# Kernel tuning notes

Measured on AMD Instinct MI355X. Metric: run time of the kernel, lower is better.

The kernel has to match this reference:

```python
import jax, jax.numpy as jnp
import numpy as np

N, E, G = 50000, 800000, 1000
F_IN, H, C = 128, 4, 64  # in-features, heads, per-head channels
NEG_SLOPE = 0.2


def _leaky_relu(v):
    return jnp.where(v > 0, v, NEG_SLOPE * v)


def _gat_conv(x, edge_index, W, a_src, a_dst, bias, heads, out_ch, concat):
    """PyG-style GATConv with add_self_loops=True (eval mode, no dropout)."""
    n = x.shape[0]
    loop = jnp.arange(n, dtype=edge_index.dtype)
    src = jnp.concatenate([edge_index[0], loop])  # [E+N]
    dst = jnp.concatenate([edge_index[1], loop])  # [E+N]
    h = (x @ W).reshape(n, heads, out_ch)          # [N, H, C]
    al_src = jnp.sum(h * a_src, axis=-1)           # [N, H]
    al_dst = jnp.sum(h * a_dst, axis=-1)           # [N, H]
    e = _leaky_relu(al_src[src] + al_dst[dst])     # [E+N, H]
    # segment softmax over incoming edges of each destination node
    m = jax.ops.segment_max(e, dst, num_segments=n)
    ex = jnp.exp(e - jax.lax.stop_gradient(m)[dst])
    denom = jax.ops.segment_sum(ex, dst, num_segments=n)
    alpha = ex / denom[dst]                        # [E+N, H]
    out = jax.ops.segment_sum(h[src] * alpha[..., None], dst, num_segments=n)
    out = out.reshape(n, heads * out_ch) if concat else out.mean(axis=1)
    return out + bias


def _global_mean_pool(x, batch, num_graphs):
    s = jax.ops.segment_sum(x, batch, num_segments=num_graphs)
    cnt = jax.ops.segment_sum(jnp.ones((x.shape[0],), x.dtype), batch, num_segments=num_graphs)
    return s / jnp.maximum(cnt, 1.0)[:, None]


def setup_inputs() -> dict:
    key = jax.random.key(0)
    ks = jax.random.split(key, 20)
    glorot = lambda k, shp: jax.random.normal(k, shp, jnp.float32) * np.sqrt(2.0 / (shp[0] + shp[-1]))
    inp = {
        "x": jax.random.normal(ks[0], (N, F_IN), jnp.float32),
        "edge_index": jax.random.randint(ks[1], (2, E), 0, N, jnp.int32),
        "batch": jnp.sort(jax.random.randint(ks[2], (N,), 0, G, jnp.int32)),
        # conv1: F_IN -> H*C (concat)
        "W1": glorot(ks[3], (F_IN, H * C)),
        "a1_src": glorot(ks[4], (H, C)),
        "a1_dst": glorot(ks[5], (H, C)),
        "b1": jnp.zeros((H * C,), jnp.float32),
        # conv2: H*C -> H*C (concat)
        "W2": glorot(ks[6], (H * C, H * C)),
        "a2_src": glorot(ks[7], (H, C)),
        "a2_dst": glorot(ks[8], (H, C)),
        "b2": jnp.zeros((H * C,), jnp.float32),
        # conv3: H*C -> C (1 head, concat=False)
        "W3": glorot(ks[9], (H * C, C)),
        "a3_src": glorot(ks[10], (1, C)),
        "a3_dst": glorot(ks[11], (1, C)),
        "b3": jnp.zeros((C,), jnp.float32),
        # final linear C -> 1
        "lin_w": glorot(ks[12], (C, 1)),
        "lin_b": jnp.zeros((1,), jnp.float32),
    }
    return inp


def reference(x, edge_index, batch, W1, a1_src, a1_dst, b1, W2, a2_src, a2_dst, b2,
              W3, a3_src, a3_dst, b3, lin_w, lin_b):
    h = jax.nn.elu(_gat_conv(x, edge_index, W1, a1_src, a1_dst, b1, H, C, True))
    h = jax.nn.elu(_gat_conv(h, edge_index, W2, a2_src, a2_dst, b2, H, C, True))
    h = _gat_conv(h, edge_index, W3, a3_src, a3_dst, b3, 1, C, False)
    g = _global_mean_pool(h, batch, G)  # [G, C]
    return g @ lin_w + lin_b            # [G, 1]
```

## Files before the change

### kernel.cpp

```cpp
#include <hip/hip_runtime.h>
#include <cstdint>
#include <cstddef>

#define NEG_SLOPE 0.2f

typedef __attribute__((ext_vector_type(8))) short short8;
typedef __attribute__((ext_vector_type(4))) float f32x4;

__device__ __forceinline__ float lrelu(float v) { return v > 0.f ? v : NEG_SLOPE * v; }

__device__ __forceinline__ unsigned short f2bf(float x) {
    unsigned u = __float_as_uint(x);
    u = (u + 0x7FFFu + ((u >> 16) & 1u)) >> 16;
    return (unsigned short)u;
}
__device__ __forceinline__ float bf2f(unsigned short h) {
    return __uint_as_float(((unsigned)h) << 16);
}

__device__ __forceinline__ void splitbf(float v, unsigned short& hb, unsigned short& lb) {
    unsigned u = __float_as_uint(v);
    hb = (unsigned short)(u >> 16);
    float hf = __uint_as_float(u & 0xFFFF0000u);
    float lf = v - hf;
    lb = (unsigned short)(__float_as_uint(lf) >> 16);
}

__global__ void k_count(const int* __restrict__ ei, int E, int* __restrict__ counts) {
    int i = blockIdx.x * blockDim.x + threadIdx.x;
    if (i < E) atomicAdd(&counts[ei[E + i]], 1);
}

__global__ __launch_bounds__(256) void k_scan_local(const int* __restrict__ counts,
        int* __restrict__ local_ex, int* __restrict__ bsums, int Nn) {
    int base = blockIdx.x * 1024;
    int tid = threadIdx.x;
    int idx = base + tid * 4;
    int4 v = make_int4(0, 0, 0, 0);
    if (idx + 3 < Nn) {
        v = *reinterpret_cast<const int4*>(&counts[idx]);
    } else {
        if (idx + 0 < Nn) v.x = counts[idx + 0];
        if (idx + 1 < Nn) v.y = counts[idx + 1];
        if (idx + 2 < Nn) v.z = counts[idx + 2];
        if (idx + 3 < Nn) v.w = counts[idx + 3];
    }
    int t = v.x + v.y + v.z + v.w;
    int lane = tid & 63, wave = tid >> 6;
    int s = t;
    #pragma unroll
    for (int off = 1; off < 64; off <<= 1) {
        int u = __shfl_up(s, off);
        if (lane >= off) s += u;
    }
    __shared__ int wsum[4];
    if (lane == 63) wsum[wave] = s;
    __syncthreads();
    int wo = 0;
    #pragma unroll
    for (int wv = 0; wv < 4; ++wv) wo += (wv < wave) ? wsum[wv] : 0;
    int ex = wo + s - t;
    int4 o;
    o.x = ex; o.y = ex + v.x; o.z = ex + v.x + v.y; o.w = ex + v.x + v.y + v.z;
    if (idx + 3 < Nn) {
        *reinterpret_cast<int4*>(&local_ex[idx]) = o;
    } else {
        if (idx + 0 < Nn) local_ex[idx + 0] = o.x;
        if (idx + 1 < Nn) local_ex[idx + 1] = o.y;
        if (idx + 2 < Nn) local_ex[idx + 2] = o.z;
        if (idx + 3 < Nn) local_ex[idx + 3] = o.w;
    }
    if (tid == 255) bsums[blockIdx.x] = wo + s;
}

__global__ __launch_bounds__(256) void k_scan_add(const int* __restrict__ local_ex,
        const int* __restrict__ bsums, int* __restrict__ indptr, int* __restrict__ cursor,
        int Nn, int Etot, int NB) {
    __shared__ int pref[64];
    int tid = threadIdx.x;
    if (tid < 64) {
        int v = (tid < NB) ? bsums[tid] : 0;
        int s = v;
        #pragma unroll
        for (int off = 1; off < 64; off <<= 1) {
            int u = __shfl_up(s, off);
            if ((tid & 63) >= off) s += u;
        }
        pref[tid] = s - v;
    }
    __syncthreads();
    int i = blockIdx.x * 256 + tid;
    if (i < Nn) {
        int val = local_ex[i] + pref[i >> 10];
        indptr[i] = val;
        cursor[i] = val;
    } else if (i == Nn) {
        indptr[Nn] = Etot;
    }
}

__global__ void k_scatter(const int* __restrict__ ei, int E, int* __restrict__ cursor,
                          int* __restrict__ csr_src) {
    int i = blockIdx.x * blockDim.x + threadIdx.x;
    if (i < E) {
        int s = ei[i], d = ei[E + i];
        int pos = atomicAdd(&cursor[d], 1);
        csr_src[pos] = s;
    }
}

__device__ __forceinline__ void packB_one(const float* __restrict__ W,
        unsigned short* __restrict__ Ph, unsigned short* __restrict__ Pl,
        int K, int M, int tid) {
    int KS8 = K >> 3;
    int col = tid / KS8;
    int k = (tid - col * KS8) << 3;
    short8 hv, lv;
    #pragma unroll
    for (int j = 0; j < 8; ++j) {
        float x = W[(size_t)(k + j) * M + col];
        unsigned short hb = f2bf(x);
        hv[j] = (short)hb;
        lv[j] = (short)f2bf(x - bf2f(hb));
    }
    int ct64 = col >> 6, c = col & 63;
    int fb = c >> 4, cl = c & 15;
    int ks = k >> 5, kg = (k >> 3) & 3;
    int lane = cl | (kg << 4);
    size_t off = (((size_t)ct64 * (K >> 5) + ks) * 4 + fb) * 64 + lane;
    *reinterpret_cast<short8*>(Ph + off * 8) = hv;
    *reinterpret_cast<short8*>(Pl + off * 8) = lv;
}

__global__ __launch_bounds__(256) void k_packB3(const float* __restrict__ W1,
        const float* __restrict__ W2, const float* __restrict__ W3,
        unsigned short* p1h, unsigned short* p1l,
        unsigned short* p2h, unsigned short* p2l,
        unsigned short* p3h, unsigned short* p3l) {
    int tid = blockIdx.x * 256 + threadIdx.x;
    if (tid < 4096)        packB_one(W1, p1h, p1l, 128, 256, tid);
    else if (tid < 12288)  packB_one(W2, p2h, p2l, 256, 256, tid - 4096);
    else if (tid < 14336)  packB_one(W3, p3h, p3l, 256, 64, tid - 12288);
}

template<int AF, int WR, int WC, bool CONV, int K>
__global__ __launch_bounds__(256) void k_mm(const float* __restrict__ A,
        const unsigned short* __restrict__ Aph, const unsigned short* __restrict__ Apl,
        const unsigned short* __restrict__ Bh, const unsigned short* __restrict__ Bl,
        unsigned short* __restrict__ C, const float* __restrict__ a_src, const float* __restrict__ a_dst,
        float* __restrict__ al_s, float* __restrict__ al_d, int Nrows, int M) {
    constexpr int BF = 4;
    constexpr int BR = WR * AF * 16;
    constexpr int KS = K >> 5;
    int wave = threadIdx.x >> 6, lane = threadIdx.x & 63;
    int wr = wave / WC, wc = wave % WC;
    int rt = blockIdx.x;
    int ct64 = blockIdx.y * WC + wc;
    int rl = lane & 15, kg = lane >> 4;
    const short8* B8h = reinterpret_cast<const short8*>(Bh);
    const short8* B8l = reinterpret_cast<const short8*>(Bl);

    const float* aptr[AF];
    const unsigned short *ahp[AF], *alp[AF];
    #pragma unroll
    for (int f = 0; f < AF; ++f) {
        int row = rt * BR + wr * (AF * 16) + f * 16 + rl;
        if (row > Nrows - 1) row = Nrows - 1;
        if constexpr (CONV) {
            aptr[f] = A + (size_t)row * K + kg * 8;
        } else {
            ahp[f] = Aph + (size_t)row * K + kg * 8;
            alp[f] = Apl + (size_t)row * K + kg * 8;
        }
    }

    f32x4 acc[AF][BF];
    #pragma unroll
    for (int i = 0; i < AF; ++i)
        #pragma unroll
        for (int j = 0; j < BF; ++j)
            acc[i][j] = (f32x4){0.f, 0.f, 0.f, 0.f};

    #pragma unroll
    for (int ks = 0; ks < KS; ++ks) {
        short8 a_h[AF], a_l[AF], b_h[BF], b_l[BF];
        #pragma unroll
        for (int f = 0; f < AF; ++f) {
            if constexpr (CONV) {
                const float* ap = aptr[f] + ks * 32;
                float4 v0 = *reinterpret_cast<const float4*>(ap);
                float4 v1 = *reinterpret_cast<const float4*>(ap + 4);
                float vv[8] = {v0.x, v0.y, v0.z, v0.w, v1.x, v1.y, v1.z, v1.w};
                #pragma unroll
                for (int j = 0; j < 8; ++j) {
                    unsigned short hb, lb;
                    splitbf(vv[j], hb, lb);
                    a_h[f][j] = (short)hb;
                    a_l[f][j] = (short)lb;
                }
            } else {
                a_h[f] = *reinterpret_cast<const short8*>(ahp[f] + ks * 32);
                a_l[f] = *reinterpret_cast<const short8*>(alp[f] + ks * 32);
            }
        }
        #pragma unroll
        for (int f = 0; f < BF; ++f) {
            size_t off = (((size_t)ct64 * KS + ks) * 4 + f) * 64 + lane;
            b_h[f] = B8h[off]; b_l[f] = B8l[off];
        }
        #pragma unroll
        for (int i = 0; i < AF; ++i)
            #pragma unroll
            for (int j = 0; j < BF; ++j) {
                acc[i][j] = __builtin_amdgcn_mfma_f32_16x16x32_bf16(a_l[i], b_h[j], acc[i][j], 0, 0, 0);
                acc[i][j] = __builtin_amdgcn_mfma_f32_16x16x32_bf16(a_h[i], b_l[j], acc[i][j], 0, 0, 0);
                acc[i][j] = __builtin_amdgcn_mfma_f32_16x16x32_bf16(a_h[i], b_h[j], acc[i][j], 0, 0, 0);
            }
    }

    int H = M >> 6;
    int head = ct64;
    int col0 = ct64 * 64;
    int cl = lane & 15, rgrp = lane >> 4;

    float as_[BF], ad_[BF];
    #pragma unroll
    for (int j = 0; j < BF; ++j) {
        as_[j] = a_src[col0 + j * 16 + cl];
        ad_[j] = a_dst[col0 + j * 16 + cl];
    }

    #pragma unroll
    for (int i = 0; i < AF; ++i) {
        int rowb = rt * BR + wr * (AF * 16) + i * 16 + rgrp * 4;
        #pragma unroll
        for (int r = 0; r < 4; ++r) {
            float sv = acc[i][0][r] * as_[0] + acc[i][1][r] * as_[1]
                     + acc[i][2][r] * as_[2] + acc[i][3][r] * as_[3];
            float dv = acc[i][0][r] * ad_[0] + acc[i][1][r] * ad_[1]
                     + acc[i][2][r] * ad_[2] + acc[i][3][r] * ad_[3];
            #pragma unroll
            for (int o = 1; o < 16; o <<= 1) {
                sv += __shfl_xor(sv, o);
                dv += __shfl_xor(dv, o);
            }
            int row = rowb + r;
            if (row < Nrows) {
                unsigned short* cp = &C[(size_t)row * M + col0 + cl];
                cp[0]  = f2bf(acc[i][0][r]);
                cp[16] = f2bf(acc[i][1][r]);
                cp[32] = f2bf(acc[i][2][r]);
                cp[48] = f2bf(acc[i][3][r]);
                if (cl == 0) {
                    al_s[(size_t)row * H + head] = sv;
                    al_d[(size_t)row * H + head] = dv;
                }
            }
        }
    }
}

template <int H, bool ACT, bool POOL>
__global__ __launch_bounds__(256) void k_agg(const unsigned short* __restrict__ hlin,
                      const float* __restrict__ al_s,
                      const float* __restrict__ al_d, const int* __restrict__ indptr,
                      const int* __restrict__ csr_src, const float* __restrict__ bias,
                      unsigned short* __restrict__ out_hi, unsigned short* __restrict__ out_lo,
                      float* __restrict__ outf, const int* __restrict__ batch,
                      int* __restrict__ gcnt, int Nn) {
    constexpr int TOT = H * 64;
    constexpr int VEC = TOT / 64;
    constexpr int CAP = 128;
    constexpr int GRPW = 64 / H;
    __shared__ float sp[4][CAP * H];
    __shared__ int   si[4][CAP];
    int w = threadIdx.x >> 6;
    int lane = threadIdx.x & 63;
    int node = (blockIdx.x * blockDim.x + threadIdx.x) >> 6;
    if (node >= Nn) return;
    int d = node;
    int p0 = indptr[d], p1 = indptr[d + 1];
    int deg = p1 - p0;
    int head = (lane * VEC) >> 6;

    float ad[H], e_self[H];
    if constexpr (H == 4) {
        float4 adv = *reinterpret_cast<const float4*>(&al_d[(size_t)d * 4]);
        float4 asv = *reinterpret_cast<const float4*>(&al_s[(size_t)d * 4]);
        ad[0] = adv.x; ad[1] = adv.y; ad[2] = adv.z; ad[3] = adv.w;
        e_self[0] = lrelu(asv.x + ad[0]); e_self[1] = lrelu(asv.y + ad[1]);
        e_self[2] = lrelu(asv.z + ad[2]); e_self[3] = lrelu(asv.w + ad[3]);
    } else {
        ad[0] = al_d[d];
        e_self[0] = lrelu(al_s[d] + ad[0]);
    }

    if (deg <= CAP) {
        int nb = (deg + 63) >> 6;
        for (int b = 0; b < nb; ++b) {
            int l = b * 64 + lane;
            float e_h[H];
            if (l < deg) {
                int s = csr_src[p0 + l];
                si[w][l] = s;
                if constexpr (H == 4) {
                    float4 sv = *reinterpret_cast<const float4*>(&al_s[(size_t)s * 4]);
                    e_h[0] = lrelu(sv.x + ad[0]); e_h[1] = lrelu(sv.y + ad[1]);
                    e_h[2] = lrelu(sv.z + ad[2]); e_h[3] = lrelu(sv.w + ad[3]);
                } else {
                    e_h[0] = lrelu(al_s[s] + ad[0]);
                }
            } else {
                #pragma unroll
                for (int h = 0; h < H; ++h) e_h[h] = -1e30f;
            }
            #pragma unroll
            for (int h = 0; h < H; ++h) sp[w][l * H + h] = e_h[h];
        }
        int li = lane & (GRPW - 1);
        int tot = nb * 64;
        float mg = e_self[head];
        for (int l = li; l < tot; l += GRPW)
            mg = fmaxf(mg, sp[w][l * H + head]);
        #pragma unroll
        for (int o = 1; o < GRPW; o <<= 1)
            mg = fmaxf(mg, __shfl_xor(mg, o));
        float deng = 0.f;
        for (int l = li; l < tot; l += GRPW) {
            float pv = __expf(sp[w][l * H + head] - mg);
            sp[w][l * H + head] = pv;
            deng += pv;
        }
        #pragma unroll
        for (int o = 1; o < GRPW; o <<= 1)
            deng += __shfl_xor(deng, o);
        float esx = __expf(e_self[head] - mg);
        deng += esx;
        float invden = 1.f / deng;

        float4 accv = make_float4(0.f, 0.f, 0.f, 0.f);
        {
            const unsigned short* hp = hlin + (size_t)d * TOT + lane * VEC;
            if constexpr (VEC == 4) {
                ushort4 hv = *reinterpret_cast<const ushort4*>(hp);
                accv.x = esx * bf2f(hv.x); accv.y = esx * bf2f(hv.y);
                accv.z = esx * bf2f(hv.z); accv.w = esx * bf2f(hv.w);
            } else {
                accv.x = esx * bf2f(hp[0]);
            }
        }
        int e = 0;
        for (; e + 8 <= deg; e += 8) {
            int s0 = si[w][e + 0], s1 = si[w][e + 1], s2 = si[w][e + 2], s3 = si[w][e + 3];
            int s4 = si[w][e + 4], s5 = si[w][e + 5], s6 = si[w][e + 6], s7 = si[w][e + 7];
            float a0 = sp[w][(e + 0) * H + head];
            float a1 = sp[w][(e + 1) * H + head];
            float a2 = sp[w][(e + 2) * H + head];
            float a3 = sp[w][(e + 3) * H + head];
            float a4 = sp[w][(e + 4) * H + head];
            float a5 = sp[w][(e + 5) * H + head];
            float a6 = sp[w][(e + 6) * H + head];
            float a7 = sp[w][(e + 7) * H + head];
            if constexpr (VEC == 4) {
                ushort4 r0 = *reinterpret_cast<const ushort4*>(hlin + (size_t)s0 * TOT + lane * 4);
                ushort4 r1 = *reinterpret_cast<const ushort4*>(hlin + (size_t)s1 * TOT + lane * 4);
                ushort4 r2 = *reinterpret_cast<const ushort4*>(hlin + (size_t)s2 * TOT + lane * 4);
                ushort4 r3 = *reinterpret_cast<const ushort4*>(hlin + (size_t)s3 * TOT + lane * 4);
                ushort4 r4 = *reinterpret_cast<const ushort4*>(hlin + (size_t)s4 * TOT + lane * 4);
                ushort4 r5 = *reinterpret_cast<const ushort4*>(hlin + (size_t)s5 * TOT + lane * 4);
                ushort4 r6 = *reinterpret_cast<const ushort4*>(hlin + (size_t)s6 * TOT + lane * 4);
                ushort4 r7 = *reinterpret_cast<const ushort4*>(hlin + (size_t)s7 * TOT + lane * 4);
                accv.x += a0*bf2f(r0.x) + a1*bf2f(r1.x) + a2*bf2f(r2.x) + a3*bf2f(r3.x)
                        + a4*bf2f(r4.x) + a5*bf2f(r5.x) + a6*bf2f(r6.x) + a7*bf2f(r7.x);
                accv.y += a0*bf2f(r0.y) + a1*bf2f(r1.y) + a2*bf2f(r2.y) + a3*bf2f(r3.y)
                        + a4*bf2f(r4.y) + a5*bf2f(r5.y) + a6*bf2f(r6.y) + a7*bf2f(r7.y);
                accv.z += a0*bf2f(r0.z) + a1*bf2f(r1.z) + a2*bf2f(r2.z) + a3*bf2f(r3.z)
                        + a4*bf2f(r4.z) + a5*bf2f(r5.z) + a6*bf2f(r6.z) + a7*bf2f(r7.z);
                accv.w += a0*bf2f(r0.w) + a1*bf2f(r1.w) + a2*bf2f(r2.w) + a3*bf2f(r3.w)
                        + a4*bf2f(r4.w) + a5*bf2f(r5.w) + a6*bf2f(r6.w) + a7*bf2f(r7.w);
            } else {
                float r0 = bf2f(hlin[(size_t)s0 * TOT + lane]);
                float r1 = bf2f(hlin[(size_t)s1 * TOT + lane]);
                float r2 = bf2f(hlin[(size_t)s2 * TOT + lane]);
                float r3 = bf2f(hlin[(size_t)s3 * TOT + lane]);
                float r4 = bf2f(hlin[(size_t)s4 * TOT + lane]);
                float r5 = bf2f(hlin[(size_t)s5 * TOT + lane]);
                float r6 = bf2f(hlin[(size_t)s6 * TOT + lane]);
                float r7 = bf2f(hlin[(size_t)s7 * TOT + lane]);
                accv.x += a0*r0 + a1*r1 + a2*r2 + a3*r3 + a4*r4 + a5*r5 + a6*r6 + a7*r7;
            }
        }
        for (; e + 4 <= deg; e += 4) {
            int s0 = si[w][e + 0], s1 = si[w][e + 1];
            int s2 = si[w][e + 2], s3 = si[w][e + 3];
            float a0 = sp[w][(e + 0) * H + head];
            float a1 = sp[w][(e + 1) * H + head];
            float a2 = sp[w][(e + 2) * H + head];
            float a3 = sp[w][(e + 3) * H + head];
            if constexpr (VEC == 4) {
                ushort4 r0 = *reinterpret_cast<const ushort4*>(hlin + (size_t)s0 * TOT + lane * 4);
                ushort4 r1 = *reinterpret_cast<const ushort4*>(hlin + (size_t)s1 * TOT + lane * 4);
                ushort4 r2 = *reinterpret_cast<const ushort4*>(hlin + (size_t)s2 * TOT + lane * 4);
                ushort4 r3 = *reinterpret_cast<const ushort4*>(hlin + (size_t)s3 * TOT + lane * 4);
                accv.x += a0*bf2f(r0.x) + a1*bf2f(r1.x) + a2*bf2f(r2.x) + a3*bf2f(r3.x);
                accv.y += a0*bf2f(r0.y) + a1*bf2f(r1.y) + a2*bf2f(r2.y) + a3*bf2f(r3.y);
                accv.z += a0*bf2f(r0.z) + a1*bf2f(r1.z) + a2*bf2f(r2.z) + a3*bf2f(r3.z);
                accv.w += a0*bf2f(r0.w) + a1*bf2f(r1.w) + a2*bf2f(r2.w) + a3*bf2f(r3.w);
            } else {
                float r0 = bf2f(hlin[(size_t)s0 * TOT + lane]);
                float r1 = bf2f(hlin[(size_t)s1 * TOT + lane]);
                float r2 = bf2f(hlin[(size_t)s2 * TOT + lane]);
                float r3 = bf2f(hlin[(size_t)s3 * TOT + lane]);
                accv.x += a0 * r0 + a1 * r1 + a2 * r2 + a3 * r3;
            }
        }
        for (; e < deg; ++e) {
            int s = si[w][e];
            float a = sp[w][e * H + head];
            if constexpr (VEC == 4) {
                ushort4 rv = *reinterpret_cast<const ushort4*>(hlin + (size_t)s * TOT + lane * 4);
                accv.x += a * bf2f(rv.x); accv.y += a * bf2f(rv.y);
                accv.z += a * bf2f(rv.z); accv.w += a * bf2f(rv.w);
            } else {
                accv.x += a * bf2f(hlin[(size_t)s * TOT + lane]);
            }
        }
        if constexpr (VEC == 4) {
            int c0 = lane * 4;
            accv.x = accv.x * invden + bias[c0 + 0];
            accv.y = accv.y * invden + bias[c0 + 1];
            accv.z = accv.z * invden + bias[c0 + 2];
            accv.w = accv.w * invden + bias[c0 + 3];
            if (ACT) {
                accv.x = accv.x > 0.f ? accv.x : expm1f(accv.x);
                accv.y = accv.y > 0.f ? accv.y : expm1f(accv.y);
                accv.z = accv.z > 0.f ? accv.z : expm1f(accv.z);
                accv.w = accv.w > 0.f ? accv.w : expm1f(accv.w);
            }
            ushort4 hv, lv;
            splitbf(accv.x, hv.x, lv.x);
            splitbf(accv.y, hv.y, lv.y);
            splitbf(accv.z, hv.z, lv.z);
            splitbf(accv.w, hv.w, lv.w);
            *reinterpret_cast<ushort4*>(&out_hi[(size_t)d * TOT + c0]) = hv;
            *reinterpret_cast<ushort4*>(&out_lo[(size_t)d * TOT + c0]) = lv;
        } else {
            float o = accv.x * invden + bias[lane];
            if (ACT) o = o > 0.f ? o : expm1f(o);
            if constexpr (POOL) {
                int g = batch[d];
                atomicAdd(&outf[(size_t)g * 64 + lane], o);
                if (lane == 0) atomicAdd(&gcnt[g], 1);
            } else {
                unsigned short hb, lb;
                splitbf(o, hb, lb);
                out_hi[(size_t)d * TOT + lane] = hb;
                out_lo[(size_t)d * TOT + lane] = lb;
            }
        }
        return;
    }

    {
        float adh = ad[head];
        float es = e_self[head];
        float m = es;
        for (int e = p0; e < p1; ++e) {
            int s = csr_src[e];
            m = fmaxf(m, lrelu(al_s[(size_t)s * H + head] + adh));
        }
        float den = __expf(es - m);
        for (int e = p0; e < p1; ++e) {
            int s = csr_src[e];
            den += __expf(lrelu(al_s[(size_t)s * H + head] + adh) - m);
        }
        den = 1.f / den;
        float accv[VEC] = {};
        {
            float alpha = __expf(es - m) * den;
            const unsigned short* hp = hlin + (size_t)d * TOT + lane * VEC;
            #pragma unroll
            for (int v = 0; v < VEC; ++v) accv[v] = alpha * bf2f(hp[v]);
        }
        for (int e = p0; e < p1; ++e) {
            int s = csr_src[e];
            float alpha = __expf(lrelu(al_s[(size_t)s * H + head] + adh) - m) * den;
            const unsigned short* hp = hlin + (size_t)s * TOT + lane * VEC;
            #pragma unroll
            for (int v = 0; v < VEC; ++v) accv[v] += alpha * bf2f(hp[v]);
        }
        #pragma unroll
        for (int v = 0; v < VEC; ++v) {
            int c = lane * VEC + v;
            float o = accv[v] + bias[c];
            if (ACT) o = o > 0.f ? o : expm1f(o);
            accv[v] = o;
        }
        if constexpr (POOL) {
            int g = batch[d];
            atomicAdd(&outf[(size_t)g * 64 + lane], accv[0]);
            if (lane == 0) atomicAdd(&gcnt[g], 1);
        } else {
            #pragma unroll
            for (int v = 0; v < VEC; ++v) {
                unsigned short hb, lb;
                splitbf(accv[v], hb, lb);
                out_hi[(size_t)d * TOT + lane * VEC + v] = hb;
                out_lo[(size_t)d * TOT + lane * VEC + v] = lb;
            }
        }
    }
}

__global__ void k_final(const float* __restrict__ gsum, const int* __restrict__ gcnt,
                        const float* __restrict__ lin_w, const float* __restrict__ lin_b,
                        float* __restrict__ out, int Gn) {
    int g = (blockIdx.x * blockDim.x + threadIdx.x) >> 6;
    int lane = threadIdx.x & 63;
    if (g >= Gn) return;
    float cnt = (float)gcnt[g];
    float inv = 1.f / fmaxf(cnt, 1.f);
    float v = gsum[(size_t)g * 64 + lane] * inv * lin_w[lane];
    #pragma unroll
    for (int off = 32; off >= 1; off >>= 1) v += __shfl_xor(v, off);
    if (lane == 0) out[g] = v + lin_b[0];
}

extern "C" void kernel_launch(void* const* d_in, const int* in_sizes, int n_in,
                              void* d_out, int out_size, void* d_ws, size_t ws_size,
                              hipStream_t stream) {
    const float* x    = (const float*)d_in[0];
    const int*   ei   = (const int*)d_in[1];
    const int*   batch= (const int*)d_in[2];
    const float* W1   = (const float*)d_in[3];
    const float* a1s  = (const float*)d_in[4];
    const float* a1d  = (const float*)d_in[5];
    const float* b1   = (const float*)d_in[6];
    const float* W2   = (const float*)d_in[7];
    const float* a2s  = (const float*)d_in[8];
    const float* a2d  = (const float*)d_in[9];
    const float* b2   = (const float*)d_in[10];
    const float* W3   = (const float*)d_in[11];
    const float* a3s  = (const float*)d_in[12];
    const float* a3d  = (const float*)d_in[13];
    const float* b3   = (const float*)d_in[14];
    const float* lw   = (const float*)d_in[15];
    const float* lb   = (const float*)d_in[16];

    int N = in_sizes[0] / 128;
    int E = in_sizes[1] / 2;
    int G = out_size;
    int RT32 = (N + 31) >> 5;
    int RT64 = (N + 63) >> 6;
    int Np = ((N + 127) >> 7) * 128;
    int NB = (N + 1023) >> 10;

    char* p = (char*)d_ws;
    auto alloc = [&](size_t bytes) {
        char* r = p;
        p += (bytes + 255) & ~(size_t)255;
        return r;
    };
    unsigned short* hbuf = (unsigned short*)alloc((size_t)Np * 256 * 2);
    unsigned short* aggh = (unsigned short*)alloc((size_t)Np * 256 * 2);
    unsigned short* aggl = (unsigned short*)alloc((size_t)Np * 256 * 2);
    unsigned short* pB1h = (unsigned short*)alloc((size_t)128 * 256 * 2);
    unsigned short* pB1l = (unsigned short*)alloc((size_t)128 * 256 * 2);
    unsigned short* pB2h = (unsigned short*)alloc((size_t)256 * 256 * 2);
    unsigned short* pB2l = (unsigned short*)alloc((size_t)256 * 256 * 2);
    unsigned short* pB3h = (unsigned short*)alloc((size_t)256 * 64 * 2);
    unsigned short* pB3l = (unsigned short*)alloc((size_t)256 * 64 * 2);
    float* al_s  = (float*)alloc((size_t)N * 4 * 4);
    float* al_d  = (float*)alloc((size_t)N * 4 * 4);
    int* indptr  = (int*)alloc((size_t)(N + 1) * 4);
    int* counts  = (int*)alloc((size_t)N * 4);
    int* cursor  = (int*)alloc((size_t)N * 4);
    int* lex     = (int*)alloc((size_t)N * 4);
    int* bsums   = (int*)alloc((size_t)256 * 4);
    int* csr     = (int*)alloc((size_t)E * 4);
    float* gsum  = (float*)alloc((size_t)G * 64 * 4);
    int* gcnt    = (int*)alloc((size_t)G * 4);
    if ((size_t)(p - (char*)d_ws) > ws_size) return;

    hipMemsetAsync(counts, 0, (size_t)N * 4, stream);
    hipMemsetAsync(gsum, 0, (size_t)G * 64 * 4, stream);
    hipMemsetAsync(gcnt, 0, (size_t)G * 4, stream);

    k_packB3<<<(14336 + 255) / 256, 256, 0, stream>>>(W1, W2, W3,
        pB1h, pB1l, pB2h, pB2l, pB3h, pB3l);

    int eb = (E + 255) / 256;
    k_count<<<eb, 256, 0, stream>>>(ei, E, counts);
    k_scan_local<<<NB, 256, 0, stream>>>(counts, lex, bsums, N);
    k_scan_add<<<(N + 1 + 255) / 256, 256, 0, stream>>>(lex, bsums, indptr, cursor, N, E, NB);
    k_scatter<<<eb, 256, 0, stream>>>(ei, E, cursor, csr);

    int wb = (N * 64 + 255) / 256;

    k_mm<2, 1, 4, true, 128><<<dim3(RT32, 1), 256, 0, stream>>>(x, nullptr, nullptr,
        pB1h, pB1l, hbuf, a1s, a1d, al_s, al_d, N, 256);
    k_agg<4, true, false><<<wb, 256, 0, stream>>>(hbuf, al_s, al_d, indptr, csr, b1,
        aggh, aggl, nullptr, nullptr, nullptr, N);

    k_mm<2, 1, 4, false, 256><<<dim3(RT32, 1), 256, 0, stream>>>(nullptr, aggh, aggl,
        pB2h, pB2l, hbuf, a2s, a2d, al_s, al_d, N, 256);
    k_agg<4, true, false><<<wb, 256, 0, stream>>>(hbuf, al_s, al_d, indptr, csr, b2,
        aggh, aggl, nullptr, nullptr, nullptr, N);

    k_mm<1, 4, 1, false, 256><<<dim3(RT64, 1), 256, 0, stream>>>(nullptr, aggh, aggl,
        pB3h, pB3l, hbuf, a3s, a3d, al_s, al_d, N, 64);
    k_agg<1, false, true><<<wb, 256, 0, stream>>>(hbuf, al_s, al_d, indptr, csr, b3,
        nullptr, nullptr, gsum, batch, gcnt, N);

    int fb = (G * 64 + 255) / 256;
    k_final<<<fb, 256, 0, stream>>>(gsum, gcnt, lw, lb, (float*)d_out, G);
}
```

Measured before the change: 407.3 us.

## Split GAT aggregation per head with head-major attention logits

The 4-head aggregation kernel is restructured so each wave handles a single (node, head) pair rather than a whole node. Blocks are ordered so consecutive blocks share a head across node pairs, and the attention logits are stored head-major (al_s[head*Npad+row]) to make per-head gathers contiguous. Within a wave, four 16-lane groups each gather a different neighbor's 64-channel head slice and combine via shuffles. The aim is to cut per-wave softmax work and improve cache locality of the gathered features. The cost is four times as many waves, each re-reading the CSR indices and neighbor logits.

```diff
diff --git a/kernel.cpp b/kernel.cpp
--- a/kernel.cpp
+++ b/kernel.cpp
@@ -148,7 +148,7 @@
         const unsigned short* __restrict__ Aph, const unsigned short* __restrict__ Apl,
         const unsigned short* __restrict__ Bh, const unsigned short* __restrict__ Bl,
         unsigned short* __restrict__ C, const float* __restrict__ a_src, const float* __restrict__ a_dst,
-        float* __restrict__ al_s, float* __restrict__ al_d, int Nrows, int M) {
+        float* __restrict__ al_s, float* __restrict__ al_d, int Nrows, int M, int Npad) {
     constexpr int BF = 4;
     constexpr int BR = WR * AF * 16;
     constexpr int KS = K >> 5;
@@ -218,7 +218,6 @@
             }
     }
 
-    int H = M >> 6;
     int head = ct64;
     int col0 = ct64 * 64;
     int cl = lane & 15, rgrp = lane >> 4;
@@ -252,263 +251,218 @@
                 cp[32] = f2bf(acc[i][2][r]);
                 cp[48] = f2bf(acc[i][3][r]);
                 if (cl == 0) {
-                    al_s[(size_t)row * H + head] = sv;
-                    al_d[(size_t)row * H + head] = dv;
+                    al_s[(size_t)head * Npad + row] = sv;
+                    al_d[(size_t)head * Npad + row] = dv;
                 }
             }
         }
     }
 }
 
-template <int H, bool ACT, bool POOL>
-__global__ __launch_bounds__(256) void k_agg(const unsigned short* __restrict__ hlin,
-                      const float* __restrict__ al_s,
-                      const float* __restrict__ al_d, const int* __restrict__ indptr,
-                      const int* __restrict__ csr_src, const float* __restrict__ bias,
-                      unsigned short* __restrict__ out_hi, unsigned short* __restrict__ out_lo,
-                      float* __restrict__ outf, const int* __restrict__ batch,
-                      int* __restrict__ gcnt, int Nn) {
-    constexpr int TOT = H * 64;
-    constexpr int VEC = TOT / 64;
+template <bool ACT>
+__global__ __launch_bounds__(256) void k_agg4(const unsigned short* __restrict__ hlin,
+        const float* __restrict__ al_s, const float* __restrict__ al_d,
+        const int* __restrict__ indptr, const int* __restrict__ csr_src,
+        const float* __restrict__ bias,
+        unsigned short* __restrict__ out_hi, unsigned short* __restrict__ out_lo,
+        int Nn, int Npad) {
     constexpr int CAP = 128;
-    constexpr int GRPW = 64 / H;
-    __shared__ float sp[4][CAP * H];
+    __shared__ float sp[4][CAP];
     __shared__ int   si[4][CAP];
     int w = threadIdx.x >> 6;
     int lane = threadIdx.x & 63;
-    int node = (blockIdx.x * blockDim.x + threadIdx.x) >> 6;
-    if (node >= Nn) return;
-    int d = node;
+    int b = blockIdx.x;
+    int r = b & 7, chunk = b >> 3;
+    int q = r >> 1;
+    int nb = chunk * 2 + (r & 1);
+    int d = nb * 4 + w;
+    if (d >= Nn) return;
     int p0 = indptr[d], p1 = indptr[d + 1];
     int deg = p1 - p0;
-    int head = (lane * VEC) >> 6;
-
-    float ad[H], e_self[H];
-    if constexpr (H == 4) {
-        float4 adv = *reinterpret_cast<const float4*>(&al_d[(size_t)d * 4]);
-        float4 asv = *reinterpret_cast<const float4*>(&al_s[(size_t)d * 4]);
-        ad[0] = adv.x; ad[1] = adv.y; ad[2] = adv.z; ad[3] = adv.w;
-        e_self[0] = lrelu(asv.x + ad[0]); e_self[1] = lrelu(asv.y + ad[1]);
-        e_self[2] = lrelu(asv.z + ad[2]); e_self[3] = lrelu(asv.w + ad[3]);
-    } else {
-        ad[0] = al_d[d];
-        e_self[0] = lrelu(al_s[d] + ad[0]);
-    }
+    float adq = al_d[(size_t)q * Npad + d];
+    float e_self = lrelu(al_s[(size_t)q * Npad + d] + adq);
+    int g = lane >> 4, li = lane & 15;
 
     if (deg <= CAP) {
-        int nb = (deg + 63) >> 6;
-        for (int b = 0; b < nb; ++b) {
-            int l = b * 64 + lane;
-            float e_h[H];
-            if (l < deg) {
-                int s = csr_src[p0 + l];
-                si[w][l] = s;
-                if constexpr (H == 4) {
-                    float4 sv = *reinterpret_cast<const float4*>(&al_s[(size_t)s * 4]);
-                    e_h[0] = lrelu(sv.x + ad[0]); e_h[1] = lrelu(sv.y + ad[1]);
-                    e_h[2] = lrelu(sv.z + ad[2]); e_h[3] = lrelu(sv.w + ad[3]);
-                } else {
-                    e_h[0] = lrelu(al_s[s] + ad[0]);
-                }
-            } else {
-                #pragma unroll
-                for (int h = 0; h < H; ++h) e_h[h] = -1e30f;
+        float m = e_self;
+        for (int l = lane; l < deg; l += 64) {
+            int s = csr_src[p0 + l];
+            si[w][l] = s;
+            float e = lrelu(al_s[(size_t)q * Npad + s] + adq);
+            sp[w][l] = e;
+            m = fmaxf(m, e);
+        }
+        #pragma unroll
+        for (int o = 1; o < 64; o <<= 1) m = fmaxf(m, __shfl_xor(m, o));
+        float den = 0.f;
+        for (int l = lane; l < deg; l += 64) {
+            float pv = __expf(sp[w][l] - m);
+            sp[w][l] = pv;
+            den += pv;
+        }
+        #pragma unroll
+        for (int o = 1; o < 64; o <<= 1) den += __shfl_xor(den, o);
+        float esx = __expf(e_self - m);
+        den += esx;
+        float invden = 1.f / den;
+
+        const unsigned short* base = hlin + q * 64 + li * 4;
+        float4 acc = make_float4(0.f, 0.f, 0.f, 0.f);
+        if (g == 0) {
+            ushort4 hv = *reinterpret_cast<const ushort4*>(base + (size_t)d * 256);
+            acc.x = esx * bf2f(hv.x); acc.y = esx * bf2f(hv.y);
+            acc.z = esx * bf2f(hv.z); acc.w = esx * bf2f(hv.w);
+        }
+        for (int e = 0; e < deg; e += 8) {
+            int e0 = e + g, e1 = e + 4 + g;
+            bool v0 = e0 < deg, v1 = e1 < deg;
+            int s0 = v0 ? si[w][e0] : d;
+            int s1 = v1 ? si[w][e1] : d;
+            float a0 = v0 ? sp[w][e0] : 0.f;
+            float a1 = v1 ? sp[w][e1] : 0.f;
+            ushort4 r0 = *reinterpret_cast<const ushort4*>(base + (size_t)s0 * 256);
+            ushort4 r1 = *reinterpret_cast<const ushort4*>(base + (size_t)s1 * 256);
+            acc.x += a0 * bf2f(r0.x) + a1 * bf2f(r1.x);
+            acc.y += a0 * bf2f(r0.y) + a1 * bf2f(r1.y);
+            acc.z += a0 * bf2f(r0.z) + a1 * bf2f(r1.z);
+            acc.w += a0 * bf2f(r0.w) + a1 * bf2f(r1.w);
+        }
+        #pragma unroll
+        for (int o = 16; o < 64; o <<= 1) {
+            acc.x += __shfl_xor(acc.x, o);
+            acc.y += __shfl_xor(acc.y, o);
+            acc.z += __shfl_xor(acc.z, o);
+            acc.w += __shfl_xor(acc.w, o);
+        }
+        if (g == 0) {
+            int c0 = q * 64 + li * 4;
+            acc.x = acc.x * invden + bias[c0 + 0];
+            acc.y = acc.y * invden + bias[c0 + 1];
+            acc.z = acc.z * invden + bias[c0 + 2];
+            acc.w = acc.w * invden + bias[c0 + 3];
+            if (ACT) {
+                acc.x = acc.x > 0.f ? acc.x : expm1f(acc.x);
+                acc.y = acc.y > 0.f ? acc.y : expm1f(acc.y);
+                acc.z = acc.z > 0.f ? acc.z : expm1f(acc.z);
+                acc.w = acc.w > 0.f ? acc.w : expm1f(acc.w);
             }
-            #pragma unroll
-            for (int h = 0; h < H; ++h) sp[w][l * H + h] = e_h[h];
-        }
-        int li = lane & (GRPW - 1);
-        int tot = nb * 64;
-        float mg = e_self[head];
-        for (int l = li; l < tot; l += GRPW)
-            mg = fmaxf(mg, sp[w][l * H + head]);
-        #pragma unroll
-        for (int o = 1; o < GRPW; o <<= 1)
-            mg = fmaxf(mg, __shfl_xor(mg, o));
-        float deng = 0.f;
-        for (int l = li; l < tot; l += GRPW) {
-            float pv = __expf(sp[w][l * H + head] - mg);
-            sp[w][l * H + head] = pv;
-            deng += pv;
-        }
-        #pragma unroll
-        for (int o = 1; o < GRPW; o <<= 1)
-            deng += __shfl_xor(deng, o);
-        float esx = __expf(e_self[head] - mg);
-        deng += esx;
-        float invden = 1.f / deng;
-
-        float4 accv = make_float4(0.f, 0.f, 0.f, 0.f);
-        {
-            const unsigned short* hp = hlin + (size_t)d * TOT + lane * VEC;
-            if constexpr (VEC == 4) {
-                ushort4 hv = *reinterpret_cast<const ushort4*>(hp);
-                accv.x = esx * bf2f(hv.x); accv.y = esx * bf2f(hv.y);
-                accv.z = esx * bf2f(hv.z); accv.w = esx * bf2f(hv.w);
-            } else {
-                accv.x = esx * bf2f(hp[0]);
-            }
-        }
+            ushort4 hv, lv;
+            splitbf(acc.x, hv.x, lv.x);
+            splitbf(acc.y, hv.y, lv.y);
+            splitbf(acc.z, hv.z, lv.z);
+            splitbf(acc.w, hv.w, lv.w);
+            *reinterpret_cast<ushort4*>(&out_hi[(size_t)d * 256 + c0]) = hv;
+            *reinterpret_cast<ushort4*>(&out_lo[(size_t)d * 256 + c0]) = lv;
+        }
+        return;
+    }
+
+    {
+        float m = e_self;
+        for (int e = p0; e < p1; ++e)
+            m = fmaxf(m, lrelu(al_s[(size_t)q * Npad + csr_src[e]] + adq));
+        float den = __expf(e_self - m);
+        for (int e = p0; e < p1; ++e)
+            den += __expf(lrelu(al_s[(size_t)q * Npad + csr_src[e]] + adq) - m);
+        float invden = 1.f / den;
+        const unsigned short* basef = hlin + q * 64 + lane;
+        float acc = __expf(e_self - m) * bf2f(basef[(size_t)d * 256]);
+        for (int e = p0; e < p1; ++e) {
+            int s = csr_src[e];
+            float a = __expf(lrelu(al_s[(size_t)q * Npad + s] + adq) - m);
+            acc += a * bf2f(basef[(size_t)s * 256]);
+        }
+        acc = acc * invden + bias[q * 64 + lane];
+        if (ACT) acc = acc > 0.f ? acc : expm1f(acc);
+        unsigned short hb, lb;
+        splitbf(acc, hb, lb);
+        out_hi[(size_t)d * 256 + q * 64 + lane] = hb;
+        out_lo[(size_t)d * 256 + q * 64 + lane] = lb;
+    }
+}
+
+__global__ __launch_bounds__(256) void k_agg1(const unsigned short* __restrict__ hlin,
+        const float* __restrict__ al_s, const float* __restrict__ al_d,
+        const int* __restrict__ indptr, const int* __restrict__ csr_src,
+        const float* __restrict__ bias, float* __restrict__ gsum,
+        const int* __restrict__ batch, int* __restrict__ gcnt, int Nn) {
+    constexpr int CAP = 128;
+    __shared__ float sp[4][CAP];
+    __shared__ int   si[4][CAP];
+    int w = threadIdx.x >> 6;
+    int lane = threadIdx.x & 63;
+    int d = (blockIdx.x * blockDim.x + threadIdx.x) >> 6;
+    if (d >= Nn) return;
+    int p0 = indptr[d], p1 = indptr[d + 1];
+    int deg = p1 - p0;
+    float adq = al_d[d];
+    float e_self = lrelu(al_s[d] + adq);
+
+    float invden, esx, m;
+    if (deg <= CAP) {
+        m = e_self;
+        for (int l = lane; l < deg; l += 64) {
+            int s = csr_src[p0 + l];
+            si[w][l] = s;
+            float e = lrelu(al_s[s] + adq);
+            sp[w][l] = e;
+            m = fmaxf(m, e);
+        }
+        #pragma unroll
+        for (int o = 1; o < 64; o <<= 1) m = fmaxf(m, __shfl_xor(m, o));
+        float den = 0.f;
+        for (int l = lane; l < deg; l += 64) {
+            float pv = __expf(sp[w][l] - m);
+            sp[w][l] = pv;
+            den += pv;
+        }
+        #pragma unroll
+        for (int o = 1; o < 64; o <<= 1) den += __shfl_xor(den, o);
+        esx = __expf(e_self - m);
+        den += esx;
+        invden = 1.f / den;
+
+        float acc = esx * bf2f(hlin[(size_t)d * 64 + lane]);
         int e = 0;
-        for (; e + 8 <= deg; e += 8) {
-            int s0 = si[w][e + 0], s1 = si[w][e + 1], s2 = si[w][e + 2], s3 = si[w][e + 3];
-            int s4 = si[w][e + 4], s5 = si[w][e + 5], s6 = si[w][e + 6], s7 = si[w][e + 7];
-            float a0 = sp[w][(e + 0) * H + head];
-            float a1 = sp[w][(e + 1) * H + head];
-            float a2 = sp[w][(e + 2) * H + head];
-            float a3 = sp[w][(e + 3) * H + head];
-            float a4 = sp[w][(e + 4) * H + head];
-            float a5 = sp[w][(e + 5) * H + head];
-            float a6 = sp[w][(e + 6) * H + head];
-            float a7 = sp[w][(e + 7) * H + head];
-            if constexpr (VEC == 4) {
-                ushort4 r0 = *reinterpret_cast<const ushort4*>(hlin + (size_t)s0 * TOT + lane * 4);
-                ushort4 r1 = *reinterpret_cast<const ushort4*>(hlin + (size_t)s1 * TOT + lane * 4);
-                ushort4 r2 = *reinterpret_cast<const ushort4*>(hlin + (size_t)s2 * TOT + lane * 4);
-                ushort4 r3 = *reinterpret_cast<const ushort4*>(hlin + (size_t)s3 * TOT + lane * 4);
-                ushort4 r4 = *reinterpret_cast<const ushort4*>(hlin + (size_t)s4 * TOT + lane * 4);
-                ushort4 r5 = *reinterpret_cast<const ushort4*>(hlin + (size_t)s5 * TOT + lane * 4);
-                ushort4 r6 = *reinterpret_cast<const ushort4*>(hlin + (size_t)s6 * TOT + lane * 4);
-                ushort4 r7 = *reinterpret_cast<const ushort4*>(hlin + (size_t)s7 * TOT + lane * 4);
-                accv.x += a0*bf2f(r0.x) + a1*bf2f(r1.x) + a2*bf2f(r2.x) + a3*bf2f(r3.x)
-                        + a4*bf2f(r4.x) + a5*bf2f(r5.x) + a6*bf2f(r6.x) + a7*bf2f(r7.x);
-                accv.y += a0*bf2f(r0.y) + a1*bf2f(r1.y) + a2*bf2f(r2.y) + a3*bf2f(r3.y)
-                        + a4*bf2f(r4.y) + a5*bf2f(r5.y) + a6*bf2f(r6.y) + a7*bf2f(r7.y);
-                accv.z += a0*bf2f(r0.z) + a1*bf2f(r1.z) + a2*bf2f(r2.z) + a3*bf2f(r3.z)
-                        + a4*bf2f(r4.z) + a5*bf2f(r5.z) + a6*bf2f(r6.z) + a7*bf2f(r7.z);
-                accv.w += a0*bf2f(r0.w) + a1*bf2f(r1.w) + a2*bf2f(r2.w) + a3*bf2f(r3.w)
-                        + a4*bf2f(r4.w) + a5*bf2f(r5.w) + a6*bf2f(r6.w) + a7*bf2f(r7.w);
-            } else {
-                float r0 = bf2f(hlin[(size_t)s0 * TOT + lane]);
-                float r1 = bf2f(hlin[(size_t)s1 * TOT + lane]);
-                float r2 = bf2f(hlin[(size_t)s2 * TOT + lane]);
-                float r3 = bf2f(hlin[(size_t)s3 * TOT + lane]);
-                float r4 = bf2f(hlin[(size_t)s4 * TOT + lane]);
-                float r5 = bf2f(hlin[(size_t)s5 * TOT + lane]);
-                float r6 = bf2f(hlin[(size_t)s6 * TOT + lane]);
-                float r7 = bf2f(hlin[(size_t)s7 * TOT + lane]);
-                accv.x += a0*r0 + a1*r1 + a2*r2 + a3*r3 + a4*r4 + a5*r5 + a6*r6 + a7*r7;
-            }
-        }
         for (; e + 4 <= deg; e += 4) {
             int s0 = si[w][e + 0], s1 = si[w][e + 1];
             int s2 = si[w][e + 2], s3 = si[w][e + 3];
-            float a0 = sp[w][(e + 0) * H + head];
-            float a1 = sp[w][(e + 1) * H + head];
-            float a2 = sp[w][(e + 2) * H + head];
-            float a3 = sp[w][(e + 3) * H + head];
-            if constexpr (VEC == 4) {
-                ushort4 r0 = *reinterpret_cast<const ushort4*>(hlin + (size_t)s0 * TOT + lane * 4);
-                ushort4 r1 = *reinterpret_cast<const ushort4*>(hlin + (size_t)s1 * TOT + lane * 4);
-                ushort4 r2 = *reinterpret_cast<const ushort4*>(hlin + (size_t)s2 * TOT + lane * 4);
-                ushort4 r3 = *reinterpret_cast<const ushort4*>(hlin + (size_t)s3 * TOT + lane * 4);
-                accv.x += a0*bf2f(r0.x) + a1*bf2f(r1.x) + a2*bf2f(r2.x) + a3*bf2f(r3.x);
-                accv.y += a0*bf2f(r0.y) + a1*bf2f(r1.y) + a2*bf2f(r2.y) + a3*bf2f(r3.y);
-                accv.z += a0*bf2f(r0.z) + a1*bf2f(r1.z) + a2*bf2f(r2.z) + a3*bf2f(r3.z);
-                accv.w += a0*bf2f(r0.w) + a1*bf2f(r1.w) + a2*bf2f(r2.w) + a3*bf2f(r3.w);
-            } else {
-                float r0 = bf2f(hlin[(size_t)s0 * TOT + lane]);
-                float r1 = bf2f(hlin[(size_t)s1 * TOT + lane]);
-                float r2 = bf2f(hlin[(size_t)s2 * TOT + lane]);
-                float r3 = bf2f(hlin[(size_t)s3 * TOT + lane]);
-                accv.x += a0 * r0 + a1 * r1 + a2 * r2 + a3 * r3;
-            }
+            float a0 = sp[w][e + 0], a1 = sp[w][e + 1];
+            float a2 = sp[w][e + 2], a3 = sp[w][e + 3];
+            float r0 = bf2f(hlin[(size_t)s0 * 64 + lane]);
+            float r1 = bf2f(hlin[(size_t)s1 * 64 + lane]);
+            float r2 = bf2f(hlin[(size_t)s2 * 64 + lane]);
+            float r3 = bf2f(hlin[(size_t)s3 * 64 + lane]);
+            acc += a0 * r0 + a1 * r1 + a2 * r2 + a3 * r3;
         }
         for (; e < deg; ++e) {
             int s = si[w][e];
-            float a = sp[w][e * H + head];
-            if constexpr (VEC == 4) {
-                ushort4 rv = *reinterpret_cast<const ushort4*>(hlin + (size_t)s * TOT + lane * 4);
-                accv.x += a * bf2f(rv.x); accv.y += a * bf2f(rv.y);
-                accv.z += a * bf2f(rv.z); accv.w += a * bf2f(rv.w);
-            } else {
-                accv.x += a * bf2f(hlin[(size_t)s * TOT + lane]);
-            }
-        }
-        if constexpr (VEC == 4) {
-            int c0 = lane * 4;
-            accv.x = accv.x * invden + bias[c0 + 0];
-            accv.y = accv.y * invden + bias[c0 + 1];
-            accv.z = accv.z * invden + bias[c0 + 2];
-            accv.w = accv.w * invden + bias[c0 + 3];
-            if (ACT) {
-                accv.x = accv.x > 0.f ? accv.x : expm1f(accv.x);
-                accv.y = accv.y > 0.f ? accv.y : expm1f(accv.y);
-                accv.z = accv.z > 0.f ? accv.z : expm1f(accv.z);
-                accv.w = accv.w > 0.f ? accv.w : expm1f(accv.w);
-            }
-            ushort4 hv, lv;
-            splitbf(accv.x, hv.x, lv.x);
-            splitbf(accv.y, hv.y, lv.y);
-            splitbf(accv.z, hv.z, lv.z);
-            splitbf(accv.w, hv.w, lv.w);
-            *reinterpret_cast<ushort4*>(&out_hi[(size_t)d * TOT + c0]) = hv;
-            *reinterpret_cast<ushort4*>(&out_lo[(size_t)d * TOT + c0]) = lv;
-        } else {
-            float o = accv.x * invden + bias[lane];
-            if (ACT) o = o > 0.f ? o : expm1f(o);
-            if constexpr (POOL) {
-                int g = batch[d];
-                atomicAdd(&outf[(size_t)g * 64 + lane], o);
-                if (lane == 0) atomicAdd(&gcnt[g], 1);
-            } else {
-                unsigned short hb, lb;
-                splitbf(o, hb, lb);
-                out_hi[(size_t)d * TOT + lane] = hb;
-                out_lo[(size_t)d * TOT + lane] = lb;
-            }
-        }
+            acc += sp[w][e] * bf2f(hlin[(size_t)s * 64 + lane]);
+        }
+        float o = acc * invden + bias[lane];
+        int gg = batch[d];
+        atomicAdd(&gsum[(size_t)gg * 64 + lane], o);
+        if (lane == 0) atomicAdd(&gcnt[gg], 1);
         return;
     }
-
     {
-        float adh = ad[head];
-        float es = e_self[head];
-        float m = es;
+        m = e_self;
+        for (int e = p0; e < p1; ++e)
+            m = fmaxf(m, lrelu(al_s[csr_src[e]] + adq));
+        float den = __expf(e_self - m);
+        for (int e = p0; e < p1; ++e)
+            den += __expf(lrelu(al_s[csr_src[e]] + adq) - m);
+        den = 1.f / den;
+        float acc = __expf(e_self - m) * bf2f(hlin[(size_t)d * 64 + lane]);
         for (int e = p0; e < p1; ++e) {
             int s = csr_src[e];
-            m = fmaxf(m, lrelu(al_s[(size_t)s * H + head] + adh));
-        }
-        float den = __expf(es - m);
-        for (int e = p0; e < p1; ++e) {
-            int s = csr_src[e];
-            den += __expf(lrelu(al_s[(size_t)s * H + head] + adh) - m);
-        }
-        den = 1.f / den;
-        float accv[VEC] = {};
-        {
-            float alpha = __expf(es - m) * den;
-            const unsigned short* hp = hlin + (size_t)d * TOT + lane * VEC;
-            #pragma unroll
-            for (int v = 0; v < VEC; ++v) accv[v] = alpha * bf2f(hp[v]);
-        }
-        for (int e = p0; e < p1; ++e) {
-            int s = csr_src[e];
-            float alpha = __expf(lrelu(al_s[(size_t)s * H + head] + adh) - m) * den;
-            const unsigned short* hp = hlin + (size_t)s * TOT + lane * VEC;
-            #pragma unroll
-            for (int v = 0; v < VEC; ++v) accv[v] += alpha * bf2f(hp[v]);
-        }
-        #pragma unroll
-        for (int v = 0; v < VEC; ++v) {
-            int c = lane * VEC + v;
-            float o = accv[v] + bias[c];
-            if (ACT) o = o > 0.f ? o : expm1f(o);
-            accv[v] = o;
-        }
-        if constexpr (POOL) {
-            int g = batch[d];
-            atomicAdd(&outf[(size_t)g * 64 + lane], accv[0]);
-            if (lane == 0) atomicAdd(&gcnt[g], 1);
-        } else {
-            #pragma unroll
-            for (int v = 0; v < VEC; ++v) {
-                unsigned short hb, lb;
-                splitbf(accv[v], hb, lb);
-                out_hi[(size_t)d * TOT + lane * VEC + v] = hb;
-                out_lo[(size_t)d * TOT + lane * VEC + v] = lb;
-            }
-        }
+            float a = __expf(lrelu(al_s[s] + adq) - m);
+            acc += a * bf2f(hlin[(size_t)s * 64 + lane]);
+        }
+        float o = acc * den + bias[lane];
+        int gg = batch[d];
+        atomicAdd(&gsum[(size_t)gg * 64 + lane], o);
+        if (lane == 0) atomicAdd(&gcnt[gg], 1);
     }
 }
 
@@ -554,6 +508,8 @@
     int RT64 = (N + 63) >> 6;
     int Np = ((N + 127) >> 7) * 128;
     int NB = (N + 1023) >> 10;
+    int NBK = (N + 3) >> 2;
+    int NBKe = (NBK + 1) & ~1;
 
     char* p = (char*)d_ws;
     auto alloc = [&](size_t bytes) {
@@ -570,8 +526,8 @@
     unsigned short* pB2l = (unsigned short*)alloc((size_t)256 * 256 * 2);
     unsigned short* pB3h = (unsigned short*)alloc((size_t)256 * 64 * 2);
     unsigned short* pB3l = (unsigned short*)alloc((size_t)256 * 64 * 2);
-    float* al_s  = (float*)alloc((size_t)N * 4 * 4);
-    float* al_d  = (float*)alloc((size_t)N * 4 * 4);
+    float* al_s  = (float*)alloc((size_t)4 * Np * 4);
+    float* al_d  = (float*)alloc((size_t)4 * Np * 4);
     int* indptr  = (int*)alloc((size_t)(N + 1) * 4);
     int* counts  = (int*)alloc((size_t)N * 4);
     int* cursor  = (int*)alloc((size_t)N * 4);
@@ -595,22 +551,23 @@
     k_scan_add<<<(N + 1 + 255) / 256, 256, 0, stream>>>(lex, bsums, indptr, cursor, N, E, NB);
     k_scatter<<<eb, 256, 0, stream>>>(ei, E, cursor, csr);
 
+    int ab4 = NBKe * 4;
     int wb = (N * 64 + 255) / 256;
 
     k_mm<2, 1, 4, true, 128><<<dim3(RT32, 1), 256, 0, stream>>>(x, nullptr, nullptr,
-        pB1h, pB1l, hbuf, a1s, a1d, al_s, al_d, N, 256);
-    k_agg<4, true, false><<<wb, 256, 0, stream>>>(hbuf, al_s, al_d, indptr, csr, b1,
-        aggh, aggl, nullptr, nullptr, nullptr, N);
+        pB1h, pB1l, hbuf, a1s, a1d, al_s, al_d, N, 256, Np);
+    k_agg4<true><<<ab4, 256, 0, stream>>>(hbuf, al_s, al_d, indptr, csr, b1,
+        aggh, aggl, N, Np);
 
     k_mm<2, 1, 4, false, 256><<<dim3(RT32, 1), 256, 0, stream>>>(nullptr, aggh, aggl,
-        pB2h, pB2l, hbuf, a2s, a2d, al_s, al_d, N, 256);
-    k_agg<4, true, false><<<wb, 256, 0, stream>>>(hbuf, al_s, al_d, indptr, csr, b2,
-        aggh, aggl, nullptr, nullptr, nullptr, N);
+        pB2h, pB2l, hbuf, a2s, a2d, al_s, al_d, N, 256, Np);
+    k_agg4<true><<<ab4, 256, 0, stream>>>(hbuf, al_s, al_d, indptr, csr, b2,
+        aggh, aggl, N, Np);
 
     k_mm<1, 4, 1, false, 256><<<dim3(RT64, 1), 256, 0, stream>>>(nullptr, aggh, aggl,
-        pB3h, pB3l, hbuf, a3s, a3d, al_s, al_d, N, 64);
-    k_agg<1, false, true><<<wb, 256, 0, stream>>>(hbuf, al_s, al_d, indptr, csr, b3,
-        nullptr, nullptr, gsum, batch, gcnt, N);
+        pB3h, pB3l, hbuf, a3s, a3d, al_s, al_d, N, 64, Np);
+    k_agg1<<<wb, 256, 0, stream>>>(hbuf, al_s, al_d, indptr, csr, b3,
+        gsum, batch, gcnt, N);
 
     int fb = (G * 64 + 255) / 256;
     k_final<<<fb, 256, 0, stream>>>(gsum, gcnt, lw, lb, (float*)d_out, G);
```

Measured after the change: 494.2 us. 21.3% more time.
